# Kernel tuning notes

Hardware: AMD Instinct MI355X
Metric: run time of the kernel (lower is better)

The kernel has to match this reference:

```python
import jax, jax.numpy as jnp
import numpy as np

N0 = 100000
N1 = 100000
K = 16
D_MODEL = 64
D_ATTN = 32
H = 4


def setup_inputs() -> dict:
    key = jax.random.key(0)
    ks = jax.random.split(key, 12)
    inp = {
        "coords0": jax.random.normal(ks[0], (N0, 3), jnp.float32),
        "coords1": jax.random.normal(ks[1], (N1, 3), jnp.float32),
        "feats0": jax.random.normal(ks[2], (N0, D_MODEL), jnp.float32),
        "feats1": jax.random.normal(ks[3], (N1, D_MODEL), jnp.float32),
        "knn_idxs": jax.random.randint(ks[4], (1, N1, K), 0, N0, jnp.int64 if jax.config.jax_enable_x64 else jnp.int32),
        # Linear params (PyTorch Linear: y = x @ W.T + b; stored here already transposed as [in, out])
        "Wq": jax.random.normal(ks[5], (D_MODEL, D_ATTN), jnp.float32) / np.sqrt(D_MODEL),
        "bq": jnp.zeros((D_ATTN,), jnp.float32),
        "Wk": jax.random.normal(ks[6], (D_MODEL + 3, D_ATTN), jnp.float32) / np.sqrt(D_MODEL + 3),
        "bk": jnp.zeros((D_ATTN,), jnp.float32),
        "Wv": jax.random.normal(ks[7], (D_MODEL + 3, D_MODEL), jnp.float32) / np.sqrt(D_MODEL + 3),
        "bv": jnp.zeros((D_MODEL,), jnp.float32),
    }
    return inp


def reference(coords0, coords1, feats0, feats1, knn_idxs, Wq, bq, Wk, bk, Wv, bv):
    idx = knn_idxs[0]  # [N1, K] neighbor indices into cloud 0
    n1, k_ = idx.shape
    dh_attn = D_ATTN // H   # per-head query/key depth
    dh_val = D_MODEL // H   # per-head value depth

    # Irregular gathers from source cloud
    g_feats = feats0[idx]                         # [N1, K, D_MODEL]
    rel = coords0[idx] - coords1[:, None, :]      # [N1, K, 3] relative coords
    kv_in = jnp.concatenate([g_feats, rel], axis=-1)  # [N1, K, D_MODEL+3]

    # Projections + head split
    q = (feats1 @ Wq + bq).reshape(n1, H, dh_attn)                    # [N1, H, dh]
    k = (kv_in @ Wk + bk).reshape(n1, k_, H, dh_attn).transpose(0, 2, 1, 3)  # [N1, H, K, dh]
    v = (kv_in @ Wv + bv).reshape(n1, k_, H, dh_val).transpose(0, 2, 1, 3)   # [N1, H, K, dv]

    # Attention over K neighbors per point
    attn = jnp.einsum('nhd,nhkd->nhk', q, k) / np.sqrt(dh_attn).astype(np.float32)
    attn = jax.nn.softmax(attn, axis=-1)          # [N1, H, K]
    out = jnp.einsum('nhk,nhkd->nhd', attn, v)    # [N1, H, dv]
    out = out.reshape(n1, -1)                     # [N1, D_MODEL]
    return out, knn_idxs
```

## Files before the change

### kernel.cpp

```cpp
#include <hip/hip_runtime.h>


using half8   = __attribute__((ext_vector_type(8))) _Float16;
using floatx4 = __attribute__((ext_vector_type(4))) float;

template<int CTRL>
__device__ __forceinline__ float dppAdd(float x) {
    int y = __builtin_amdgcn_update_dpp(0, __float_as_int(x), CTRL, 0xF, 0xF, true);
    return x + __int_as_float(y);
}
__device__ __forceinline__ float rowSum16(float x) {
    x = dppAdd<0x121>(x);
    x = dppAdd<0x122>(x);
    x = dppAdd<0x124>(x);
    x = dppAdd<0x128>(x);
    return x;
}

__global__ __launch_bounds__(256) void prep_weights(
    const float* __restrict__ Wq, const float* __restrict__ Wk,
    const float* __restrict__ Wv,
    _Float16* __restrict__ fragKV, _Float16* __restrict__ fragQ)
{
    const int base = blockIdx.x * 256 + threadIdx.x;
    for (int e = base; e < 6144; e += 2048) {
        int j = e & 7, ln = (e >> 3) & 63, h = (e >> 9) & 1, t = e >> 10;
        int k = h * 32 + ((ln >> 4) * 8) + j;
        int n = t * 16 + (ln & 15);
        float v = (n < 32) ? Wk[k * 32 + n] : Wv[k * 64 + (n - 32)];
        fragKV[e] = (_Float16)v;
    }
    for (int e = base; e < 2048; e += 2048) {
        int j = e & 7, ln = (e >> 3) & 63, h = (e >> 9) & 1, t = e >> 10;
        int k = h * 32 + ((ln >> 4) * 8) + j;
        int n = t * 16 + (ln & 15);
        fragQ[e] = (_Float16)Wq[k * 32 + n];
    }
}

__global__ __launch_bounds__(256, 4) void proj_fused(
    const float* __restrict__ feats0, const float* __restrict__ feats1,
    const _Float16* __restrict__ fragKV, const _Float16* __restrict__ fragQ,
    const float* __restrict__ bq, const float* __restrict__ bk,
    const float* __restrict__ bv,
    _Float16* __restrict__ KVh, float* __restrict__ Qf,
    int n0, int n1, int nb0)
{
    __shared__ __align__(16) _Float16 sFrag[6144];
    __shared__ __align__(16) _Float16 sOut[6144];

    const int tid  = threadIdx.x;
    const int wave = tid >> 6;
    const int lane = tid & 63;
    const int l15  = lane & 15;
    const int quad = lane >> 4;

    if ((int)blockIdx.x < nb0) {
        const int rowBase = blockIdx.x * 64;
        half8* sF8 = (half8*)sFrag;
        const half8* fk8 = (const half8*)fragKV;
        for (int c = tid; c < 768; c += 256) sF8[c] = fk8[c];
        __syncthreads();

        const int m0   = rowBase + wave * 16;
        const int row  = m0 + l15;
        const int rowc = (row < n0) ? row : (n0 - 1);
        const floatx4* X4 = (const floatx4*)(feats0 + (size_t)rowc * 64);
        floatx4 f0 = X4[quad * 2 + 0], f1 = X4[quad * 2 + 1];
        floatx4 f2 = X4[quad * 2 + 8], f3 = X4[quad * 2 + 9];
        half8 a0, a1;
        a0[0]=(_Float16)f0.x; a0[1]=(_Float16)f0.y; a0[2]=(_Float16)f0.z; a0[3]=(_Float16)f0.w;
        a0[4]=(_Float16)f1.x; a0[5]=(_Float16)f1.y; a0[6]=(_Float16)f1.z; a0[7]=(_Float16)f1.w;
        a1[0]=(_Float16)f2.x; a1[1]=(_Float16)f2.y; a1[2]=(_Float16)f2.z; a1[3]=(_Float16)f2.w;
        a1[4]=(_Float16)f3.x; a1[5]=(_Float16)f3.y; a1[6]=(_Float16)f3.z; a1[7]=(_Float16)f3.w;

        const half8* bf = (const half8*)sFrag;
        floatx4 acc[6];
        #pragma unroll
        for (int t = 0; t < 6; t++) {
            int n = t * 16 + l15;
            float bb = (n < 32) ? bk[n] : bv[n - 32];
            acc[t] = (floatx4){bb, bb, bb, bb};
        }
        #pragma unroll
        for (int t = 0; t < 6; t++) {
            acc[t] = __builtin_amdgcn_mfma_f32_16x16x32_f16(a0, bf[(t*2+0)*64 + lane], acc[t], 0,0,0);
            acc[t] = __builtin_amdgcn_mfma_f32_16x16x32_f16(a1, bf[(t*2+1)*64 + lane], acc[t], 0,0,0);
        }

        #pragma unroll
        for (int t = 0; t < 6; t++)
            #pragma unroll
            for (int r = 0; r < 4; r++)
                sOut[(wave * 16 + quad * 4 + r) * 96 + t * 16 + l15] = (_Float16)acc[t][r];
        __syncthreads();

        const half8* so8 = (const half8*)sOut;
        half8* dst = (half8*)(KVh + (size_t)rowBase * 96);
        for (int c = tid; c < 768; c += 256) {
            int r = c / 12;
            if (rowBase + r < n0) dst[c] = so8[c];
        }
    } else {
        const int rowBase = ((int)blockIdx.x - nb0) * 64;
        half8* sF8 = (half8*)sFrag;
        const half8* fq8 = (const half8*)fragQ;
        for (int c = tid; c < 256; c += 256) sF8[c] = fq8[c];
        __syncthreads();

        const int m0   = rowBase + wave * 16;
        const int row  = m0 + l15;
        const int rowc = (row < n1) ? row : (n1 - 1);
        const floatx4* X4 = (const floatx4*)(feats1 + (size_t)rowc * 64);
        floatx4 f0 = X4[quad * 2 + 0], f1 = X4[quad * 2 + 1];
        floatx4 f2 = X4[quad * 2 + 8], f3 = X4[quad * 2 + 9];
        half8 a0, a1;
        a0[0]=(_Float16)f0.x; a0[1]=(_Float16)f0.y; a0[2]=(_Float16)f0.z; a0[3]=(_Float16)f0.w;
        a0[4]=(_Float16)f1.x; a0[5]=(_Float16)f1.y; a0[6]=(_Float16)f1.z; a0[7]=(_Float16)f1.w;
        a1[0]=(_Float16)f2.x; a1[1]=(_Float16)f2.y; a1[2]=(_Float16)f2.z; a1[3]=(_Float16)f2.w;
        a1[4]=(_Float16)f3.x; a1[5]=(_Float16)f3.y; a1[6]=(_Float16)f3.z; a1[7]=(_Float16)f3.w;

        const half8* bf = (const half8*)sFrag;
        floatx4 acc[2];
        #pragma unroll
        for (int t = 0; t < 2; t++) {
            float bb = bq[t * 16 + l15];
            acc[t] = (floatx4){bb, bb, bb, bb};
        }
        #pragma unroll
        for (int t = 0; t < 2; t++) {
            acc[t] = __builtin_amdgcn_mfma_f32_16x16x32_f16(a0, bf[(t*2+0)*64 + lane], acc[t], 0,0,0);
            acc[t] = __builtin_amdgcn_mfma_f32_16x16x32_f16(a1, bf[(t*2+1)*64 + lane], acc[t], 0,0,0);
        }
        #pragma unroll
        for (int t = 0; t < 2; t++)
            #pragma unroll
            for (int r = 0; r < 4; r++) {
                int ro = m0 + quad * 4 + r;
                if (ro < n1) Qf[(size_t)ro * 32 + t * 16 + l15] = acc[t][r];
            }
    }
}

__global__ __launch_bounds__(256, 4) void attn_kernel(
    const float* __restrict__ coords0, const float* __restrict__ coords1,
    const int*   __restrict__ knn,
    const float* __restrict__ Qf, const _Float16* __restrict__ KVh,
    const float* __restrict__ Wk, const float* __restrict__ Wv,
    float* __restrict__ out, float* __restrict__ outIdx, int n1)
{
    __shared__ __align__(16) float sQ[16][36];
    __shared__ float sWk3[3][32];
    __shared__ float sWv3[3][64];
    __shared__ __align__(16) float sT[16][12];
    __shared__ __align__(16) int   sIdx[16][16];
    __shared__ __align__(16) float sA[16][68];

    const int tid = threadIdx.x;
    for (int e = tid; e < 288; e += 256) {
        if (e < 96) ((float*)sWk3)[e] = Wk[2048 + e];
        else        ((float*)sWv3)[e - 96] = Wv[4096 + (e - 96)];
    }
    if (tid < 128) {
        int pt = tid >> 3, c4 = tid & 7;
        int r = blockIdx.x * 16 + pt;
        if (r >= n1) r = n1 - 1;
        ((floatx4*)&sQ[pt][0])[c4] = ((const floatx4*)Qf)[(size_t)r * 8 + c4];
    }
    __syncthreads();

    const int p = tid >> 4;
    const int j = tid & 15;
    const int n = blockIdx.x * 16 + p;
    const bool valid = (n < n1);
    const int nc = valid ? n : (n1 - 1);

    const int idx = knn[nc * 16 + j];

    const half8* kr = (const half8*)(KVh + (size_t)idx * 96);
    half8 k8_0 = kr[0], k8_1 = kr[1], k8_2 = kr[2], k8_3 = kr[3];

    const float r0 = coords0[idx * 3 + 0] - coords1[nc * 3 + 0];
    const float r1 = coords0[idx * 3 + 1] - coords1[nc * 3 + 1];
    const float r2 = coords0[idx * 3 + 2] - coords1[nc * 3 + 2];

    const int g    = j & 7;
    const int hf   = j >> 3;
    const int h    = g >> 1;
    const int slot = ((j & 1) << 3) + (j >> 1);

    sIdx[p][slot] = idx;

    if (j < 12) {
        int c = j >> 2, h2 = j & 3;
        float t = 0.f;
        #pragma unroll
        for (int i = 0; i < 8; i++)
            t = fmaf(sWk3[c][h2 * 8 + i], sQ[p][h2 * 8 + i], t);
        sT[p][j] = t;
    }

    const int4* si4 = (const int4*)&sIdx[p][hf * 8];
    int4 viA = si4[0], viB = si4[1];
    int vIdx[8] = {viA.x, viA.y, viA.z, viA.w, viB.x, viB.y, viB.z, viB.w};
    half8 v8[8];
    #pragma unroll
    for (int s = 0; s < 8; s++)
        v8[s] = *(const half8*)(KVh + (size_t)vIdx[s] * 96 + 32 + g * 8);

    const floatx4* t4 = (const floatx4*)&sT[p][0];
    floatx4 tc0 = t4[0], tc1 = t4[1], tc2 = t4[2];

    const float scale = 0.35355339059327373f;
    float a_h[4];
    {
        half8 k8[4] = {k8_0, k8_1, k8_2, k8_3};
        #pragma unroll
        for (int h2 = 0; h2 < 4; h2++) {
            floatx4 q0 = ((const floatx4*)&sQ[p][0])[h2 * 2 + 0];
            floatx4 q1 = ((const floatx4*)&sQ[p][0])[h2 * 2 + 1];
            float acc = r0 * tc0[h2] + r1 * tc1[h2] + r2 * tc2[h2];
            acc = fmaf(q0[0], (float)k8[h2][0], acc);
            acc = fmaf(q0[1], (float)k8[h2][1], acc);
            acc = fmaf(q0[2], (float)k8[h2][2], acc);
            acc = fmaf(q0[3], (float)k8[h2][3], acc);
            acc = fmaf(q1[0], (float)k8[h2][4], acc);
            acc = fmaf(q1[1], (float)k8[h2][5], acc);
            acc = fmaf(q1[2], (float)k8[h2][6], acc);
            acc = fmaf(q1[3], (float)k8[h2][7], acc);
            float e = __expf(acc * scale);
            float ssum = rowSum16(e);
            a_h[h2] = e * __builtin_amdgcn_rcpf(ssum);
        }
    }

    sA[p][0 * 16 + slot] = a_h[0];
    sA[p][1 * 16 + slot] = a_h[1];
    sA[p][2 * 16 + slot] = a_h[2];
    sA[p][3 * 16 + slot] = a_h[3];

    if (valid) outIdx[n * 16 + j] = (float)idx;

    float rbs0, rbs1, rbs2;
    {
        float s00 = rowSum16(a_h[0] * r0), s01 = rowSum16(a_h[1] * r0);
        float s02 = rowSum16(a_h[2] * r0), s03 = rowSum16(a_h[3] * r0);
        rbs0 = (h == 0) ? s00 : (h == 1) ? s01 : (h == 2) ? s02 : s03;
        float s10 = rowSum16(a_h[0] * r1), s11 = rowSum16(a_h[1] * r1);
        float s12 = rowSum16(a_h[2] * r1), s13 = rowSum16(a_h[3] * r1);
        rbs1 = (h == 0) ? s10 : (h == 1) ? s11 : (h == 2) ? s12 : s13;
        float s20 = rowSum16(a_h[0] * r2), s21 = rowSum16(a_h[1] * r2);
        float s22 = rowSum16(a_h[2] * r2), s23 = rowSum16(a_h[3] * r2);
        rbs2 = (h == 0) ? s20 : (h == 1) ? s21 : (h == 2) ? s22 : s23;
    }

    const floatx4* a4 = (const floatx4*)&sA[p][h * 16 + hf * 8];
    floatx4 aw0 = a4[0], aw1 = a4[1];
    float av[8] = {aw0[0], aw0[1], aw0[2], aw0[3], aw1[0], aw1[1], aw1[2], aw1[3]};

    float acc8[8] = {0,0,0,0,0,0,0,0};
    #pragma unroll
    for (int s = 0; s < 8; s++)
        #pragma unroll
        for (int i = 0; i < 8; i++)
            acc8[i] = fmaf(av[s], (float)v8[s][i], acc8[i]);

    #pragma unroll
    for (int i = 0; i < 8; i++) acc8[i] = dppAdd<0x128>(acc8[i]);

    #pragma unroll
    for (int i = 0; i < 8; i++)
        acc8[i] += rbs0 * sWv3[0][8 * g + i] + rbs1 * sWv3[1][8 * g + i] + rbs2 * sWv3[2][8 * g + i];

    if (valid) {
        floatx4 st = { acc8[hf * 4 + 0], acc8[hf * 4 + 1], acc8[hf * 4 + 2], acc8[hf * 4 + 3] };
        ((floatx4*)out)[(size_t)n * 16 + g * 2 + hf] = st;
    }
}

extern "C" void kernel_launch(void* const* d_in, const int* in_sizes, int n_in,
                              void* d_out, int out_size, void* d_ws, size_t ws_size,
                              hipStream_t stream) {
    const float* coords0 = (const float*)d_in[0];
    const float* coords1 = (const float*)d_in[1];
    const float* feats0  = (const float*)d_in[2];
    const float* feats1  = (const float*)d_in[3];
    const int*   knn     = (const int*)d_in[4];
    const float* Wq      = (const float*)d_in[5];
    const float* bq      = (const float*)d_in[6];
    const float* Wk      = (const float*)d_in[7];
    const float* bk      = (const float*)d_in[8];
    const float* Wv      = (const float*)d_in[9];
    const float* bv      = (const float*)d_in[10];

    const int n0 = in_sizes[0] / 3;
    const int n1 = in_sizes[1] / 3;

    char* ws = (char*)d_ws;
    _Float16* KVh = (_Float16*)ws;
    float*    Qf  = (float*)(ws + (size_t)n0 * 96 * 2);
    _Float16* fragKV = (_Float16*)(ws + (size_t)n0 * 96 * 2 + (size_t)n1 * 32 * 4);
    _Float16* fragQ  = fragKV + 6144;

    float* out    = (float*)d_out;
    float* outIdx = out + (size_t)n1 * 64;

    const int nb0 = (n0 + 63) / 64;
    const int nb1 = (n1 + 63) / 64;

    prep_weights<<<8, 256, 0, stream>>>(Wq, Wk, Wv, fragKV, fragQ);
    proj_fused<<<nb0 + nb1, 256, 0, stream>>>(feats0, feats1, fragKV, fragQ,
                                              bq, bk, bv, KVh, Qf, n0, n1, nb0);
    attn_kernel<<<(n1 + 15) / 16, 256, 0, stream>>>(coords0, coords1, knn,
                                                    Qf, KVh, Wk, Wv, out, outIdx, n1);
}
```

Before: 188.5 us.

## Make projection kernel persistent with grid-stride tiles and per-wave output stores

The projection kernel now launches a fixed grid of 512 KV blocks and 256 Q blocks that loop over 64-row tiles, so weight fragments and biases are loaded into shared memory once per block instead of once per tile. The block-wide barrier before the KV store is removed: each wave writes its own 16-row slice of shared memory and copies it straight to global memory. This reduces repeated weight staging and barrier cost, but relies on each wave reading back only its own shared-memory slice. It also gives up some latency hiding from the much larger grid.

Result: no change. 189.3 us (+0.4%).

```diff
diff --git a/kernel.cpp b/kernel.cpp
--- a/kernel.cpp
+++ b/kernel.cpp
@@ -44,7 +44,7 @@
     const float* __restrict__ bq, const float* __restrict__ bk,
     const float* __restrict__ bv,
     _Float16* __restrict__ KVh, float* __restrict__ Qf,
-    int n0, int n1, int nb0)
+    int n0, int n1, int nbKV, int nbQ, int tiles0, int tiles1)
 {
     __shared__ __align__(16) _Float16 sFrag[6144];
     __shared__ __align__(16) _Float16 sOut[6144];
@@ -54,91 +54,101 @@
     const int lane = tid & 63;
     const int l15  = lane & 15;
     const int quad = lane >> 4;
-
-    if ((int)blockIdx.x < nb0) {
-        const int rowBase = blockIdx.x * 64;
+    const int bid  = (int)blockIdx.x;
+
+    if (bid < nbKV) {
         half8* sF8 = (half8*)sFrag;
         const half8* fk8 = (const half8*)fragKV;
         for (int c = tid; c < 768; c += 256) sF8[c] = fk8[c];
         __syncthreads();
-
-        const int m0   = rowBase + wave * 16;
-        const int row  = m0 + l15;
-        const int rowc = (row < n0) ? row : (n0 - 1);
-        const floatx4* X4 = (const floatx4*)(feats0 + (size_t)rowc * 64);
-        floatx4 f0 = X4[quad * 2 + 0], f1 = X4[quad * 2 + 1];
-        floatx4 f2 = X4[quad * 2 + 8], f3 = X4[quad * 2 + 9];
-        half8 a0, a1;
-        a0[0]=(_Float16)f0.x; a0[1]=(_Float16)f0.y; a0[2]=(_Float16)f0.z; a0[3]=(_Float16)f0.w;
-        a0[4]=(_Float16)f1.x; a0[5]=(_Float16)f1.y; a0[6]=(_Float16)f1.z; a0[7]=(_Float16)f1.w;
-        a1[0]=(_Float16)f2.x; a1[1]=(_Float16)f2.y; a1[2]=(_Float16)f2.z; a1[3]=(_Float16)f2.w;
-        a1[4]=(_Float16)f3.x; a1[5]=(_Float16)f3.y; a1[6]=(_Float16)f3.z; a1[7]=(_Float16)f3.w;
-
         const half8* bf = (const half8*)sFrag;
-        floatx4 acc[6];
+
+        float bb[6];
         #pragma unroll
         for (int t = 0; t < 6; t++) {
             int n = t * 16 + l15;
-            float bb = (n < 32) ? bk[n] : bv[n - 32];
-            acc[t] = (floatx4){bb, bb, bb, bb};
+            bb[t] = (n < 32) ? bk[n] : bv[n - 32];
         }
-        #pragma unroll
-        for (int t = 0; t < 6; t++) {
-            acc[t] = __builtin_amdgcn_mfma_f32_16x16x32_f16(a0, bf[(t*2+0)*64 + lane], acc[t], 0,0,0);
-            acc[t] = __builtin_amdgcn_mfma_f32_16x16x32_f16(a1, bf[(t*2+1)*64 + lane], acc[t], 0,0,0);
-        }
-
-        #pragma unroll
-        for (int t = 0; t < 6; t++)
-            #pragma unroll
-            for (int r = 0; r < 4; r++)
-                sOut[(wave * 16 + quad * 4 + r) * 96 + t * 16 + l15] = (_Float16)acc[t][r];
-        __syncthreads();
-
-        const half8* so8 = (const half8*)sOut;
-        half8* dst = (half8*)(KVh + (size_t)rowBase * 96);
-        for (int c = tid; c < 768; c += 256) {
-            int r = c / 12;
-            if (rowBase + r < n0) dst[c] = so8[c];
+
+        for (int tile = bid; tile < tiles0; tile += nbKV) {
+            const int rowBase = tile * 64;
+            const int m0   = rowBase + wave * 16;
+            const int row  = m0 + l15;
+            const int rowc = (row < n0) ? row : (n0 - 1);
+            const floatx4* X4 = (const floatx4*)(feats0 + (size_t)rowc * 64);
+            floatx4 f0 = X4[quad * 2 + 0], f1 = X4[quad * 2 + 1];
+            floatx4 f2 = X4[quad * 2 + 8], f3 = X4[quad * 2 + 9];
+            half8 a0, a1;
+            a0[0]=(_Float16)f0.x; a0[1]=(_Float16)f0.y; a0[2]=(_Float16)f0.z; a0[3]=(_Float16)f0.w;
+            a0[4]=(_Float16)f1.x; a0[5]=(_Float16)f1.y; a0[6]=(_Float16)f1.z; a0[7]=(_Float16)f1.w;
+            a1[0]=(_Float16)f2.x; a1[1]=(_Float16)f2.y; a1[2]=(_Float16)f2.z; a1[3]=(_Float16)f2.w;
+            a1[4]=(_Float16)f3.x; a1[5]=(_Float16)f3.y; a1[6]=(_Float16)f3.z; a1[7]=(_Float16)f3.w;
+
+            floatx4 acc[6];
+            #pragma unroll
+            for (int t = 0; t < 6; t++) acc[t] = (floatx4){bb[t], bb[t], bb[t], bb[t]};
+            #pragma unroll
+            for (int t = 0; t < 6; t++) {
+                acc[t] = __builtin_amdgcn_mfma_f32_16x16x32_f16(a0, bf[(t*2+0)*64 + lane], acc[t], 0,0,0);
+                acc[t] = __builtin_amdgcn_mfma_f32_16x16x32_f16(a1, bf[(t*2+1)*64 + lane], acc[t], 0,0,0);
+            }
+
+            #pragma unroll
+            for (int t = 0; t < 6; t++)
+                #pragma unroll
+                for (int r = 0; r < 4; r++)
+                    sOut[(wave * 16 + quad * 4 + r) * 96 + t * 16 + l15] = (_Float16)acc[t][r];
+
+            const half8* so8 = (const half8*)sOut + wave * 192;
+            half8* dst = (half8*)(KVh + (size_t)rowBase * 96) + wave * 192;
+            #pragma unroll
+            for (int u = 0; u < 3; u++) {
+                int c = lane + u * 64;
+                int r = c / 12;
+                if (m0 + r < n0) dst[c] = so8[c];
+            }
         }
     } else {
-        const int rowBase = ((int)blockIdx.x - nb0) * 64;
         half8* sF8 = (half8*)sFrag;
         const half8* fq8 = (const half8*)fragQ;
         for (int c = tid; c < 256; c += 256) sF8[c] = fq8[c];
         __syncthreads();
-
-        const int m0   = rowBase + wave * 16;
-        const int row  = m0 + l15;
-        const int rowc = (row < n1) ? row : (n1 - 1);
-        const floatx4* X4 = (const floatx4*)(feats1 + (size_t)rowc * 64);
-        floatx4 f0 = X4[quad * 2 + 0], f1 = X4[quad * 2 + 1];
-        floatx4 f2 = X4[quad * 2 + 8], f3 = X4[quad * 2 + 9];
-        half8 a0, a1;
-        a0[0]=(_Float16)f0.x; a0[1]=(_Float16)f0.y; a0[2]=(_Float16)f0.z; a0[3]=(_Float16)f0.w;
-        a0[4]=(_Float16)f1.x; a0[5]=(_Float16)f1.y; a0[6]=(_Float16)f1.z; a0[7]=(_Float16)f1.w;
-        a1[0]=(_Float16)f2.x; a1[1]=(_Float16)f2.y; a1[2]=(_Float16)f2.z; a1[3]=(_Float16)f2.w;
-        a1[4]=(_Float16)f3.x; a1[5]=(_Float16)f3.y; a1[6]=(_Float16)f3.z; a1[7]=(_Float16)f3.w;
-
         const half8* bf = (const half8*)sFrag;
-        floatx4 acc[2];
-        #pragma unroll
-        for (int t = 0; t < 2; t++) {
-            float bb = bq[t * 16 + l15];
-            acc[t] = (floatx4){bb, bb, bb, bb};
+
+        float bb[2];
+        #pragma unroll
+        for (int t = 0; t < 2; t++) bb[t] = bq[t * 16 + l15];
+
+        for (int tile = bid - nbKV; tile < tiles1; tile += nbQ) {
+            const int rowBase = tile * 64;
+            const int m0   = rowBase + wave * 16;
+            const int row  = m0 + l15;
+            const int rowc = (row < n1) ? row : (n1 - 1);
+            const floatx4* X4 = (const floatx4*)(feats1 + (size_t)rowc * 64);
+            floatx4 f0 = X4[quad * 2 + 0], f1 = X4[quad * 2 + 1];
+            floatx4 f2 = X4[quad * 2 + 8], f3 = X4[quad * 2 + 9];
+            half8 a0, a1;
+            a0[0]=(_Float16)f0.x; a0[1]=(_Float16)f0.y; a0[2]=(_Float16)f0.z; a0[3]=(_Float16)f0.w;
+            a0[4]=(_Float16)f1.x; a0[5]=(_Float16)f1.y; a0[6]=(_Float16)f1.z; a0[7]=(_Float16)f1.w;
+            a1[0]=(_Float16)f2.x; a1[1]=(_Float16)f2.y; a1[2]=(_Float16)f2.z; a1[3]=(_Float16)f2.w;
+            a1[4]=(_Float16)f3.x; a1[5]=(_Float16)f3.y; a1[6]=(_Float16)f3.z; a1[7]=(_Float16)f3.w;
+
+            floatx4 acc[2];
+            #pragma unroll
+            for (int t = 0; t < 2; t++) acc[t] = (floatx4){bb[t], bb[t], bb[t], bb[t]};
+            #pragma unroll
+            for (int t = 0; t < 2; t++) {
+                acc[t] = __builtin_amdgcn_mfma_f32_16x16x32_f16(a0, bf[(t*2+0)*64 + lane], acc[t], 0,0,0);
+                acc[t] = __builtin_amdgcn_mfma_f32_16x16x32_f16(a1, bf[(t*2+1)*64 + lane], acc[t], 0,0,0);
+            }
+            #pragma unroll
+            for (int t = 0; t < 2; t++)
+                #pragma unroll
+                for (int r = 0; r < 4; r++) {
+                    int ro = m0 + quad * 4 + r;
+                    if (ro < n1) Qf[(size_t)ro * 32 + t * 16 + l15] = acc[t][r];
+                }
         }
-        #pragma unroll
-        for (int t = 0; t < 2; t++) {
-            acc[t] = __builtin_amdgcn_mfma_f32_16x16x32_f16(a0, bf[(t*2+0)*64 + lane], acc[t], 0,0,0);
-            acc[t] = __builtin_amdgcn_mfma_f32_16x16x32_f16(a1, bf[(t*2+1)*64 + lane], acc[t], 0,0,0);
-        }
-        #pragma unroll
-        for (int t = 0; t < 2; t++)
-            #pragma unroll
-            for (int r = 0; r < 4; r++) {
-                int ro = m0 + quad * 4 + r;
-                if (ro < n1) Qf[(size_t)ro * 32 + t * 16 + l15] = acc[t][r];
-            }
     }
 }
 
@@ -305,12 +315,14 @@
     float* out    = (float*)d_out;
     float* outIdx = out + (size_t)n1 * 64;
 
-    const int nb0 = (n0 + 63) / 64;
-    const int nb1 = (n1 + 63) / 64;
+    const int tiles0 = (n0 + 63) / 64;
+    const int tiles1 = (n1 + 63) / 64;
+    const int nbKV = 512, nbQ = 256;
 
     prep_weights<<<8, 256, 0, stream>>>(Wq, Wk, Wv, fragKV, fragQ);
-    proj_fused<<<nb0 + nb1, 256, 0, stream>>>(feats0, feats1, fragKV, fragQ,
-                                              bq, bk, bv, KVh, Qf, n0, n1, nb0);
+    proj_fused<<<nbKV + nbQ, 256, 0, stream>>>(feats0, feats1, fragKV, fragQ,
+                                               bq, bk, bv, KVh, Qf,
+                                               n0, n1, nbKV, nbQ, tiles0, tiles1);
     attn_kernel<<<(n1 + 15) / 16, 256, 0, stream>>>(coords0, coords1, knn,
                                                     Qf, KVh, Wk, Wv, out, outIdx, n1);
 }
```
